# Kernel tuning notes

Hardware: AMD Instinct MI355X
Metric: run time of the kernel (lower is better)

The kernel has to match this reference:

```python
import jax, jax.numpy as jnp
from jax import lax
import numpy as np

B, T, F_IN, H = 64, 128, 12, 128  # batch, seq_len, input/output features, hidden


def _uinit(key, shape, fan):
    return jax.random.uniform(key, shape, jnp.float32, -1.0, 1.0) / np.float32(np.sqrt(fan))


def setup_inputs() -> dict:
    key = jax.random.key(0)
    ks = jax.random.split(key, 12)
    inp = {
        "x": jax.random.normal(ks[0], (B, T, F_IN), jnp.float32),
        # encoder LSTM (gate order i,f,g,o; b = b_ih + b_hh folded together)
        "enc_Wih": _uinit(ks[1], (4 * H, F_IN), H),
        "enc_Whh": _uinit(ks[2], (4 * H, H), H),
        "enc_b": _uinit(ks[3], (4 * H,), H),
        # decoder LSTM (input is the 12-dim teacher-forced x slice)
        "dec_Wih": _uinit(ks[4], (4 * H, F_IN), H),
        "dec_Whh": _uinit(ks[5], (4 * H, H), H),
        "dec_b": _uinit(ks[6], (4 * H,), H),
        # attention: Linear(2H -> H) with bias, then v: Linear(H -> 1, no bias)
        "attn_W": _uinit(ks[7], (H, 2 * H), 2 * H),
        "attn_b": _uinit(ks[8], (H,), 2 * H),
        "v_w": _uinit(ks[9], (H,), H),
        # output layer: Linear(2H -> F_IN)  (intended width; see notes)
        "out_W": _uinit(ks[10], (F_IN, 2 * H), 2 * H),
        "out_b": _uinit(ks[11], (F_IN,), 2 * H),
    }
    return inp


def _lstm_cell(xt, h, c, Wih, Whh, b):
    z = xt @ Wih.T + h @ Whh.T + b  # [B, 4H]
    i, f, g, o = jnp.split(z, 4, axis=-1)
    c = jax.nn.sigmoid(f) * c + jax.nn.sigmoid(i) * jnp.tanh(g)
    h = jax.nn.sigmoid(o) * jnp.tanh(c)
    return h, c


def reference(x, enc_Wih, enc_Whh, enc_b, dec_Wih, dec_Whh, dec_b,
              attn_W, attn_b, v_w, out_W, out_b):
    b_, t_, _ = x.shape
    hdim = enc_Whh.shape[1]
    xs = jnp.swapaxes(x, 0, 1)  # [T, B, F]
    h0 = jnp.zeros((b_, hdim), x.dtype)
    c0 = jnp.zeros((b_, hdim), x.dtype)

    def enc_step(carry, xt):
        h, c = carry
        h, c = _lstm_cell(xt, h, c, enc_Wih, enc_Whh, enc_b)
        return (h, c), h

    (hT, cT), enc_hs = lax.scan(enc_step, (h0, c0), xs)
    enc_out = jnp.swapaxes(enc_hs, 0, 1)  # [B, T, H]

    # split attn weight: cat(hidden, enc_out) @ W.T == hidden@W1.T + enc_out@W2.T
    W1, W2 = attn_W[:, :hdim], attn_W[:, hdim:]
    enc_proj = jnp.einsum("bth,gh->btg", enc_out, W2)  # precompute encoder side

    def dec_step(carry, xt):
        h, c = carry
        h, c = _lstm_cell(xt, h, c, dec_Wih, dec_Whh, dec_b)
        energy = jnp.tanh((h @ W1.T)[:, None, :] + enc_proj + attn_b)  # [B,T,H]
        score = jnp.einsum("bth,h->bt", energy, v_w)
        w = jax.nn.softmax(score, axis=1)  # attention over encoder time
        ctx = jnp.einsum("bt,bth->bh", w, enc_out)
        return (h, c), jnp.concatenate([h, ctx], axis=-1)  # [B, 2H]

    _, dec_ys = lax.scan(dec_step, (hT, cT), xs)
    dec_out = jnp.swapaxes(dec_ys, 0, 1)  # [B, T, 2H]
    return dec_out @ out_W.T + out_b  # [B, T, F]
```

## Files before the change

### kernel.cpp

```cpp
#include <hip/hip_runtime.h>
#include <hip/hip_bf16.h>

#define BB 64
#define TT 128
#define FIN 12
#define HH 128
#define GG 512

#define LOG2E 1.4426950408889634f
#define TWO_LOG2E 2.8853900817779268f

__device__ __forceinline__ float fexp2(float x) { return __builtin_amdgcn_exp2f(x); }
__device__ __forceinline__ float frcp(float x)  { return __builtin_amdgcn_rcpf(x); }

__device__ __forceinline__ float tanh_f(float x) {
  return 1.0f - 2.0f * frcp(1.0f + fexp2(TWO_LOG2E * x));
}
__device__ __forceinline__ float sigm_f(float x) {
  return frcp(1.0f + fexp2(-LOG2E * x));
}

template <int CTRL>
__device__ __forceinline__ float dpp_addstage(float v) {
  int s = __builtin_amdgcn_update_dpp(0, __float_as_int(v), CTRL, 0xF, 0xF, true);
  return v + __int_as_float(s);
}
__device__ __forceinline__ float red8(float v) {
  v = dpp_addstage<0xB1>(v);
  v = dpp_addstage<0x4E>(v);
  v = dpp_addstage<0x141>(v);
  return v;
}

#define FMA4S(acc, s, v) do { \
  acc.x = fmaf((s), (v).x, acc.x); \
  acc.y = fmaf((s), (v).y, acc.y); \
  acc.z = fmaf((s), (v).z, acc.z); \
  acc.w = fmaf((s), (v).w, acc.w); } while (0)

#define ACC4(hv, wv, a) do { \
  a = fmaf((hv).x, (wv).x, a); a = fmaf((hv).y, (wv).y, a); \
  a = fmaf((hv).z, (wv).z, a); a = fmaf((hv).w, (wv).w, a); } while (0)

__global__ __launch_bounds__(1024, 4) void lstm_kernel(
    const float* __restrict__ x,
    const float* __restrict__ eWih, const float* __restrict__ eWhh, const float* __restrict__ eb,
    const float* __restrict__ dWih, const float* __restrict__ dWhh, const float* __restrict__ db,
    float* __restrict__ encH, float* __restrict__ decH)
{
  const int b   = blockIdx.x;
  const int tid = threadIdx.x;
  const int q   = tid & 7;
  const int i   = tid >> 3;

  __shared__ __align__(16) float xs[TT * FIN];
  __shared__ __align__(16) float hbuf[2][160];
  __shared__ __align__(16) float hist[64 * HH];

  if (tid < (TT * FIN / 4))
    ((float4*)xs)[tid] = ((const float4*)(x + (size_t)b * TT * FIN))[tid];
  if (tid < 320) ((float*)hbuf)[tid] = 0.0f;
  float c = 0.0f;

  const int xo   = (q < 4) ? 3 * q : 0;
  const float xz = (q < 4) ? 1.0f : 0.0f;

  int ts = 0;
  #pragma unroll 1
  for (int phase = 0; phase < 2; ++phase) {
    const float* Wih  = phase ? dWih : eWih;
    const float* Whh  = phase ? dWhh : eWhh;
    const float* bias = phase ? db : eb;
    float* Hout       = phase ? decH : encH;

    float4 wg[4][4];
    #pragma unroll
    for (int g = 0; g < 4; ++g)
      #pragma unroll
      for (int j = 0; j < 4; ++j)
        wg[g][j] = *(const float4*)(Whh + ((g * HH + i) * HH) + 16 * q + 4 * j);

    float wx[4][3];
    #pragma unroll
    for (int g = 0; g < 4; ++g)
      #pragma unroll
      for (int j = 0; j < 3; ++j)
        wx[g][j] = Wih[(g * HH + i) * FIN + xo + j] * xz;

    const float bi = bias[i], bf = bias[HH + i], bg = bias[2 * HH + i], bo = bias[3 * HH + i];

    #pragma unroll 1
    for (int half = 0; half < 2; ++half) {
      #pragma unroll 1
      for (int tt = 0; tt < 64; ++tt, ++ts) {
        const int t = half * 64 + tt;
        __syncthreads();
        const float* hb = hbuf[ts & 1] + q * 20;
        float4 h0 = *(const float4*)(hb + 0);
        float4 h1 = *(const float4*)(hb + 4);
        float4 h2 = *(const float4*)(hb + 8);
        float4 h3 = *(const float4*)(hb + 12);

        const float* xt = xs + t * FIN + xo;
        float x0 = xt[0], x1 = xt[1], x2 = xt[2];
        float ai = wx[0][0] * x0 + wx[0][1] * x1 + wx[0][2] * x2;
        float af = wx[1][0] * x0 + wx[1][1] * x1 + wx[1][2] * x2;
        float ag = wx[2][0] * x0 + wx[2][1] * x1 + wx[2][2] * x2;
        float ao = wx[3][0] * x0 + wx[3][1] * x1 + wx[3][2] * x2;

        ACC4(h0, wg[0][0], ai); ACC4(h0, wg[1][0], af); ACC4(h0, wg[2][0], ag); ACC4(h0, wg[3][0], ao);
        ACC4(h1, wg[0][1], ai); ACC4(h1, wg[1][1], af); ACC4(h1, wg[2][1], ag); ACC4(h1, wg[3][1], ao);
        ACC4(h2, wg[0][2], ai); ACC4(h2, wg[1][2], af); ACC4(h2, wg[2][2], ag); ACC4(h2, wg[3][2], ao);
        ACC4(h3, wg[0][3], ai); ACC4(h3, wg[1][3], af); ACC4(h3, wg[2][3], ag); ACC4(h3, wg[3][3], ao);

        ai = red8(ai); af = red8(af); ag = red8(ag); ao = red8(ao);

        if (q == 0) {
          float zi = sigm_f(ai + bi);
          float zf = sigm_f(af + bf);
          float zg = tanh_f(ag + bg);
          float zo = sigm_f(ao + bo);
          c = fmaf(zf, c, zi * zg);
          float hn = zo * tanh_f(c);
          hbuf[(ts + 1) & 1][(i >> 4) * 20 + (i & 15)] = hn;
          hist[tt * HH + i] = hn;
        }
      }
      __syncthreads();
      {
        float4* dst = (float4*)(Hout + ((size_t)b * TT + half * 64) * HH);
        const float4* src = (const float4*)hist;
        dst[tid]        = src[tid];
        dst[tid + 1024] = src[tid + 1024];
      }
    }
  }
}

__global__ __launch_bounds__(256, 2) void proj_kernel(
    const float* __restrict__ encH, const float* __restrict__ decH,
    const float* __restrict__ attnW, const float* __restrict__ attnb,
    float* __restrict__ Abuf, float* __restrict__ Pbuf)
{
  const int m  = blockIdx.x & 1;
  const int b  = (blockIdx.x >> 1) & 63;
  const int r0 = (blockIdx.x >> 7) * 16;
  const int tid = threadIdx.x;

  __shared__ __align__(16) float WT[64 * 128];
  __shared__ __align__(16) float Xt[16 * 128];

  const float* X = (m ? encH : decH) + ((size_t)b * TT + r0) * HH;
  const float* W = attnW + (m ? HH : 0);

  ((float4*)Xt)[tid]       = ((const float4*)X)[tid];
  ((float4*)Xt)[256 + tid] = ((const float4*)X)[256 + tid];

  const int hq = tid & 31, rr = tid >> 5;
  const int h0 = 4 * hq;

  float4 acc0, acc1;
  if (m == 0) { acc0 = *(const float4*)(attnb + h0); acc1 = acc0; }
  else        { acc0 = make_float4(0.f, 0.f, 0.f, 0.f); acc1 = acc0; }

  for (int kb = 0; kb < 2; ++kb) {
    __syncthreads();
    {
      int h = tid >> 1, koff = (tid & 1) * 32;
      #pragma unroll
      for (int j = 0; j < 8; ++j) {
        float4 v = *(const float4*)(W + h * 256 + kb * 64 + koff + 4 * j);
        int kp = koff + 4 * j;
        WT[(kp + 0) * 128 + h] = v.x;
        WT[(kp + 1) * 128 + h] = v.y;
        WT[(kp + 2) * 128 + h] = v.z;
        WT[(kp + 3) * 128 + h] = v.w;
      }
    }
    __syncthreads();
    const float* xr0 = Xt + (2 * rr) * 128 + kb * 64;
    const float* xr1 = xr0 + 128;
    #pragma unroll
    for (int k4 = 0; k4 < 64; k4 += 4) {
      float4 xa = *(const float4*)(xr0 + k4);
      float4 xb = *(const float4*)(xr1 + k4);
      float4 w0 = *(const float4*)&WT[(k4 + 0) * 128 + h0];
      float4 w1 = *(const float4*)&WT[(k4 + 1) * 128 + h0];
      float4 w2 = *(const float4*)&WT[(k4 + 2) * 128 + h0];
      float4 w3 = *(const float4*)&WT[(k4 + 3) * 128 + h0];
      FMA4S(acc0, xa.x, w0); FMA4S(acc0, xa.y, w1);
      FMA4S(acc0, xa.z, w2); FMA4S(acc0, xa.w, w3);
      FMA4S(acc1, xb.x, w0); FMA4S(acc1, xb.y, w1);
      FMA4S(acc1, xb.z, w2); FMA4S(acc1, xb.w, w3);
    }
  }
  float* O = (m ? Pbuf : Abuf) + ((size_t)b * TT + r0) * HH;
  *(float4*)(O + (2 * rr) * 128 + h0)     = acc0;
  *(float4*)(O + (2 * rr + 1) * 128 + h0) = acc1;
}

__global__ __launch_bounds__(512, 2) void attn_kernel(
    const float* __restrict__ encH, const float* __restrict__ decH,
    const float* __restrict__ Abuf, const float* __restrict__ Pbuf,
    const float* __restrict__ vw, const float* __restrict__ outW,
    const float* __restrict__ outb, float* __restrict__ out)
{
  const int b  = blockIdx.x >> 3;
  const int s0 = (blockIdx.x & 7) * 16;
  const int tid = threadIdx.x;

  __shared__ __align__(16) float buf[64 * 128];
  __shared__ __align__(16) float a_lds[16 * 128];
  __shared__ __align__(16) float sc[16 * 128];
  __shared__ __align__(16) float dh[16 * 128];
  __shared__ __align__(16) float vl[HH];

  ((float4*)a_lds)[tid] = ((const float4*)(Abuf + ((size_t)b * TT + s0) * HH))[tid];
  ((float4*)dh)[tid]    = ((const float4*)(decH + ((size_t)b * TT + s0) * HH))[tid];
  if (tid < 32) ((float4*)vl)[tid] = ((const float4*)vw)[tid];

  const int u  = tid & 31;
  const int sl = tid >> 5;
  const int uq = u & 15;
  const int uh = u >> 4;

  for (int half = 0; half < 2; ++half) {
    const int tbase = half * 64;
    __syncthreads();
    #pragma unroll
    for (int i = 0; i < 4; ++i) {
      int flat = i * 2048 + tid * 4;
      int tp = flat >> 7;
      int h0 = flat & 127;
      float4 v = *(const float4*)(Pbuf + ((size_t)b * TT + tbase + tp) * HH + h0);
      int tq = tp >> 2, tr = tp & 3;
      buf[(h0 + 0) * 64 + 4 * ((tq ^ ((h0 + 0) >> 2)) & 15) + tr] = v.x;
      buf[(h0 + 1) * 64 + 4 * ((tq ^ ((h0 + 1) >> 2)) & 15) + tr] = v.y;
      buf[(h0 + 2) * 64 + 4 * ((tq ^ ((h0 + 2) >> 2)) & 15) + tr] = v.z;
      buf[(h0 + 3) * 64 + 4 * ((tq ^ ((h0 + 3) >> 2)) & 15) + tr] = v.w;
    }
    __syncthreads();
    float4 acc = make_float4(0.f, 0.f, 0.f, 0.f);
    const float* arow = a_lds + sl * 128;
    #pragma unroll 8
    for (int hh = 0; hh < 64; ++hh) {
      int h = uh * 64 + hh;
      float ah = arow[h];
      float vh = vl[h];
      float4 p4 = *(const float4*)&buf[h * 64 + 4 * ((uq ^ ((h >> 2) & 15)) & 15)];
      acc.x = fmaf(vh, tanh_f(ah + p4.x), acc.x);
      acc.y = fmaf(vh, tanh_f(ah + p4.y), acc.y);
      acc.z = fmaf(vh, tanh_f(ah + p4.z), acc.z);
      acc.w = fmaf(vh, tanh_f(ah + p4.w), acc.w);
    }
    acc.x += __shfl_xor(acc.x, 16, 64);
    acc.y += __shfl_xor(acc.y, 16, 64);
    acc.z += __shfl_xor(acc.z, 16, 64);
    acc.w += __shfl_xor(acc.w, 16, 64);
    if (uh == 0) *(float4*)&sc[sl * 128 + tbase + 4 * uq] = acc;
  }
  __syncthreads();

  {
    float4 sv = *(const float4*)&sc[sl * 128 + 4 * u];
    float mx = fmaxf(fmaxf(sv.x, sv.y), fmaxf(sv.z, sv.w));
    #pragma unroll
    for (int msk = 1; msk <= 16; msk <<= 1) mx = fmaxf(mx, __shfl_xor(mx, msk, 64));
    float4 e;
    e.x = fexp2(LOG2E * (sv.x - mx));
    e.y = fexp2(LOG2E * (sv.y - mx));
    e.z = fexp2(LOG2E * (sv.z - mx));
    e.w = fexp2(LOG2E * (sv.w - mx));
    float sm = (e.x + e.y) + (e.z + e.w);
    #pragma unroll
    for (int msk = 1; msk <= 16; msk <<= 1) sm += __shfl_xor(sm, msk, 64);
    float r = frcp(sm);
    e.x *= r; e.y *= r; e.z *= r; e.w *= r;
    *(float4*)&sc[sl * 128 + 4 * u] = e;
  }

  float4 ctx = make_float4(0.f, 0.f, 0.f, 0.f);
  const int h0c = 4 * u;
  for (int half = 0; half < 2; ++half) {
    const int tbase = half * 64;
    __syncthreads();
    #pragma unroll
    for (int i = 0; i < 4; ++i) {
      int flat = i * 2048 + tid * 4;
      int tp = flat >> 7;
      int hh0 = flat & 127;
      *(float4*)&buf[tp * 128 + hh0] =
          *(const float4*)(encH + ((size_t)b * TT + tbase + tp) * HH + hh0);
    }
    __syncthreads();
    const float* wrow = sc + sl * 128 + tbase;
    #pragma unroll 8
    for (int tp = 0; tp < 64; ++tp) {
      float wt = wrow[tp];
      float4 e4 = *(const float4*)&buf[tp * 128 + h0c];
      FMA4S(ctx, wt, e4);
    }
  }
  __syncthreads();
  *(float4*)&a_lds[sl * 128 + h0c] = ctx;
  __syncthreads();

  if (tid < 192) {
    int s = tid / 12, f = tid % 12;
    float acc = outb[f];
    const float4* w4 = (const float4*)(outW + f * 256);
    const float4* d4 = (const float4*)(dh + s * 128);
    const float4* c4 = (const float4*)(a_lds + s * 128);
    #pragma unroll
    for (int k = 0; k < 32; ++k) {
      float4 wv = w4[k], dv = d4[k];
      acc = fmaf(wv.x, dv.x, acc); acc = fmaf(wv.y, dv.y, acc);
      acc = fmaf(wv.z, dv.z, acc); acc = fmaf(wv.w, dv.w, acc);
    }
    #pragma unroll
    for (int k = 0; k < 32; ++k) {
      float4 wv = w4[32 + k], cv = c4[k];
      acc = fmaf(wv.x, cv.x, acc); acc = fmaf(wv.y, cv.y, acc);
      acc = fmaf(wv.z, cv.z, acc); acc = fmaf(wv.w, cv.w, acc);
    }
    out[((size_t)b * TT + s0 + s) * FIN + f] = acc;
  }
}

extern "C" void kernel_launch(void* const* d_in, const int* in_sizes, int n_in,
                              void* d_out, int out_size, void* d_ws, size_t ws_size,
                              hipStream_t stream)
{
  const float* x     = (const float*)d_in[0];
  const float* eWih  = (const float*)d_in[1];
  const float* eWhh  = (const float*)d_in[2];
  const float* eb    = (const float*)d_in[3];
  const float* dWih  = (const float*)d_in[4];
  const float* dWhh  = (const float*)d_in[5];
  const float* db    = (const float*)d_in[6];
  const float* attnW = (const float*)d_in[7];
  const float* attnb = (const float*)d_in[8];
  const float* vw    = (const float*)d_in[9];
  const float* outW  = (const float*)d_in[10];
  const float* outb  = (const float*)d_in[11];
  float* out = (float*)d_out;

  float* ws   = (float*)d_ws;
  const size_t SEG = (size_t)BB * TT * HH;
  float* encH = ws;
  float* decH = ws + SEG;
  float* Abuf = ws + 2 * SEG;
  float* Pbuf = ws + 3 * SEG;

  lstm_kernel<<<64, 1024, 0, stream>>>(x, eWih, eWhh, eb, dWih, dWhh, db, encH, decH);
  proj_kernel<<<1024, 256, 0, stream>>>(encH, decH, attnW, attnb, Abuf, Pbuf);
  attn_kernel<<<512, 512, 0, stream>>>(encH, decH, Abuf, Pbuf, vw, outW, outb, out);
}
```

Baseline: 338.8 us.

## Remap LSTM recurrence to one thread per gate row with quad broadcast

The recurrent LSTM kernel now assigns each of 512 threads a full gate row (128 weights held in registers) instead of splitting each hidden unit's four gates across 8 threads with DPP reductions. The cross-lane reduction is replaced by a single activation per thread, and the i/f/g/o values are then shared within each group of four lanes by DPP quad broadcasts. The intent is to shorten the serial per-timestep critical path (fewer reduction stages, parallel gate activations) and halve the block size. The cost is 128 weight registers per thread, which risks spills and lower occupancy, and every thread now reads the whole h vector from LDS (a broadcast read) each step.

```diff
diff --git a/kernel.cpp b/kernel.cpp
--- a/kernel.cpp
+++ b/kernel.cpp
@@ -21,15 +21,9 @@
 }
 
 template <int CTRL>
-__device__ __forceinline__ float dpp_addstage(float v) {
-  int s = __builtin_amdgcn_update_dpp(0, __float_as_int(v), CTRL, 0xF, 0xF, true);
-  return v + __int_as_float(s);
-}
-__device__ __forceinline__ float red8(float v) {
-  v = dpp_addstage<0xB1>(v);
-  v = dpp_addstage<0x4E>(v);
-  v = dpp_addstage<0x141>(v);
-  return v;
+__device__ __forceinline__ float quad_bcast(float v) {
+  return __int_as_float(
+      __builtin_amdgcn_update_dpp(0, __float_as_int(v), CTRL, 0xF, 0xF, true));
 }
 
 #define FMA4S(acc, s, v) do { \
@@ -42,7 +36,7 @@
   a = fmaf((hv).x, (wv).x, a); a = fmaf((hv).y, (wv).y, a); \
   a = fmaf((hv).z, (wv).z, a); a = fmaf((hv).w, (wv).w, a); } while (0)
 
-__global__ __launch_bounds__(1024, 4) void lstm_kernel(
+__global__ __launch_bounds__(512, 2) void lstm_kernel(
     const float* __restrict__ x,
     const float* __restrict__ eWih, const float* __restrict__ eWhh, const float* __restrict__ eb,
     const float* __restrict__ dWih, const float* __restrict__ dWhh, const float* __restrict__ db,
@@ -50,20 +44,20 @@
 {
   const int b   = blockIdx.x;
   const int tid = threadIdx.x;
-  const int q   = tid & 7;
-  const int i   = tid >> 3;
+  const int g   = tid & 3;
+  const int i   = tid >> 2;
 
   __shared__ __align__(16) float xs[TT * FIN];
-  __shared__ __align__(16) float hbuf[2][160];
+  __shared__ __align__(16) float hbuf[2][HH];
   __shared__ __align__(16) float hist[64 * HH];
 
   if (tid < (TT * FIN / 4))
     ((float4*)xs)[tid] = ((const float4*)(x + (size_t)b * TT * FIN))[tid];
-  if (tid < 320) ((float*)hbuf)[tid] = 0.0f;
+  if (tid < 256) ((float*)hbuf)[tid] = 0.0f;
   float c = 0.0f;
 
-  const int xo   = (q < 4) ? 3 * q : 0;
-  const float xz = (q < 4) ? 1.0f : 0.0f;
+  const bool isg = (g == 2);
+  const float mk = isg ? TWO_LOG2E : -LOG2E;
 
   int ts = 0;
   #pragma unroll 1
@@ -73,21 +67,16 @@
     const float* bias = phase ? db : eb;
     float* Hout       = phase ? decH : encH;
 
-    float4 wg[4][4];
-    #pragma unroll
-    for (int g = 0; g < 4; ++g)
-      #pragma unroll
-      for (int j = 0; j < 4; ++j)
-        wg[g][j] = *(const float4*)(Whh + ((g * HH + i) * HH) + 16 * q + 4 * j);
-
-    float wx[4][3];
-    #pragma unroll
-    for (int g = 0; g < 4; ++g)
-      #pragma unroll
-      for (int j = 0; j < 3; ++j)
-        wx[g][j] = Wih[(g * HH + i) * FIN + xo + j] * xz;
-
-    const float bi = bias[i], bf = bias[HH + i], bg = bias[2 * HH + i], bo = bias[3 * HH + i];
+    const int row = g * HH + i;
+    float4 wr[32];
+    #pragma unroll
+    for (int j = 0; j < 32; ++j)
+      wr[j] = *(const float4*)(Whh + (size_t)row * HH + 4 * j);
+
+    float4 wx0 = *(const float4*)(Wih + row * FIN + 0);
+    float4 wx1 = *(const float4*)(Wih + row * FIN + 4);
+    float4 wx2 = *(const float4*)(Wih + row * FIN + 8);
+    const float bb_ = bias[row];
 
     #pragma unroll 1
     for (int half = 0; half < 2; ++half) {
@@ -95,34 +84,42 @@
       for (int tt = 0; tt < 64; ++tt, ++ts) {
         const int t = half * 64 + tt;
         __syncthreads();
-        const float* hb = hbuf[ts & 1] + q * 20;
-        float4 h0 = *(const float4*)(hb + 0);
-        float4 h1 = *(const float4*)(hb + 4);
-        float4 h2 = *(const float4*)(hb + 8);
-        float4 h3 = *(const float4*)(hb + 12);
-
-        const float* xt = xs + t * FIN + xo;
-        float x0 = xt[0], x1 = xt[1], x2 = xt[2];
-        float ai = wx[0][0] * x0 + wx[0][1] * x1 + wx[0][2] * x2;
-        float af = wx[1][0] * x0 + wx[1][1] * x1 + wx[1][2] * x2;
-        float ag = wx[2][0] * x0 + wx[2][1] * x1 + wx[2][2] * x2;
-        float ao = wx[3][0] * x0 + wx[3][1] * x1 + wx[3][2] * x2;
-
-        ACC4(h0, wg[0][0], ai); ACC4(h0, wg[1][0], af); ACC4(h0, wg[2][0], ag); ACC4(h0, wg[3][0], ao);
-        ACC4(h1, wg[0][1], ai); ACC4(h1, wg[1][1], af); ACC4(h1, wg[2][1], ag); ACC4(h1, wg[3][1], ao);
-        ACC4(h2, wg[0][2], ai); ACC4(h2, wg[1][2], af); ACC4(h2, wg[2][2], ag); ACC4(h2, wg[3][2], ao);
-        ACC4(h3, wg[0][3], ai); ACC4(h3, wg[1][3], af); ACC4(h3, wg[2][3], ag); ACC4(h3, wg[3][3], ao);
-
-        ai = red8(ai); af = red8(af); ag = red8(ag); ao = red8(ao);
-
-        if (q == 0) {
-          float zi = sigm_f(ai + bi);
-          float zf = sigm_f(af + bf);
-          float zg = tanh_f(ag + bg);
-          float zo = sigm_f(ao + bo);
-          c = fmaf(zf, c, zi * zg);
-          float hn = zo * tanh_f(c);
-          hbuf[(ts + 1) & 1][(i >> 4) * 20 + (i & 15)] = hn;
+        const float* hb = hbuf[ts & 1];
+
+        float a0 = 0.f, a1 = 0.f, a2 = 0.f, a3 = 0.f;
+        #pragma unroll
+        for (int j = 0; j < 8; ++j) {
+          float4 h0 = *(const float4*)(hb + 16 * j + 0);
+          float4 h1 = *(const float4*)(hb + 16 * j + 4);
+          float4 h2 = *(const float4*)(hb + 16 * j + 8);
+          float4 h3 = *(const float4*)(hb + 16 * j + 12);
+          ACC4(h0, wr[4 * j + 0], a0);
+          ACC4(h1, wr[4 * j + 1], a1);
+          ACC4(h2, wr[4 * j + 2], a2);
+          ACC4(h3, wr[4 * j + 3], a3);
+        }
+        const float* xt = xs + t * FIN;
+        float4 xv0 = *(const float4*)(xt + 0);
+        float4 xv1 = *(const float4*)(xt + 4);
+        float4 xv2 = *(const float4*)(xt + 8);
+        ACC4(xv0, wx0, a0);
+        ACC4(xv1, wx1, a1);
+        ACC4(xv2, wx2, a2);
+
+        float a = ((a0 + a1) + (a2 + a3)) + bb_;
+
+        float r = frcp(1.0f + fexp2(mk * a));
+        float z = isg ? fmaf(-2.0f, r, 1.0f) : r;
+
+        float zi = quad_bcast<0x00>(z);
+        float zf = quad_bcast<0x55>(z);
+        float zg = quad_bcast<0xAA>(z);
+        float zo = quad_bcast<0xFF>(z);
+
+        c = fmaf(zf, c, zi * zg);
+        float hn = zo * tanh_f(c);
+        if (g == 0) {
+          hbuf[(ts + 1) & 1][i] = hn;
           hist[tt * HH + i] = hn;
         }
       }
@@ -131,7 +128,9 @@
         float4* dst = (float4*)(Hout + ((size_t)b * TT + half * 64) * HH);
         const float4* src = (const float4*)hist;
         dst[tid]        = src[tid];
+        dst[tid + 512]  = src[tid + 512];
         dst[tid + 1024] = src[tid + 1024];
+        dst[tid + 1536] = src[tid + 1536];
       }
     }
   }
@@ -352,7 +351,7 @@
   float* Abuf = ws + 2 * SEG;
   float* Pbuf = ws + 3 * SEG;
 
-  lstm_kernel<<<64, 1024, 0, stream>>>(x, eWih, eWhh, eb, dWih, dWhh, db, encH, decH);
+  lstm_kernel<<<64, 512, 0, stream>>>(x, eWih, eWhh, eb, dWih, dWhh, db, encH, decH);
   proj_kernel<<<1024, 256, 0, stream>>>(encH, decH, attnW, attnb, Abuf, Pbuf);
   attn_kernel<<<512, 512, 0, stream>>>(encH, decH, Abuf, Pbuf, vw, outW, outb, out);
 }
```

New measurement: 411.9 us. +21.6%, slower.

## Factor tanh exponentials into precomputed per-operand exp2 for attention energy

Applied to the files above, without the earlier changes.

Rewrites tanh(a+p) as 1 - 2/(1+e^{2a}·e^{2p}) and precomputes exp2 of both the decoder projection and the encoder projection once when they are loaded into LDS. The inner score loop then needs only one fma and one rcp per element instead of an exp2 per element. The constant term sum(v) is dropped because softmax is shift-invariant, and the score is scaled by -2. It also pads the a_lds/sc row stride to 132 and vectorizes the inner loop to read four h values per iteration. The cost is overflow risk when exp(2x) reaches inf for large projections, plus some accuracy loss.

```diff
diff --git a/kernel.cpp b/kernel.cpp
--- a/kernel.cpp
+++ b/kernel.cpp
@@ -199,6 +199,8 @@
   *(float4*)(O + (2 * rr + 1) * 128 + h0) = acc1;
 }
 
+#define AST 132
+
 __global__ __launch_bounds__(512, 2) void attn_kernel(
     const float* __restrict__ encH, const float* __restrict__ decH,
     const float* __restrict__ Abuf, const float* __restrict__ Pbuf,
@@ -210,13 +212,21 @@
   const int tid = threadIdx.x;
 
   __shared__ __align__(16) float buf[64 * 128];
-  __shared__ __align__(16) float a_lds[16 * 128];
-  __shared__ __align__(16) float sc[16 * 128];
+  __shared__ __align__(16) float a_lds[16 * AST];
+  __shared__ __align__(16) float sc[16 * AST];
   __shared__ __align__(16) float dh[16 * 128];
   __shared__ __align__(16) float vl[HH];
 
-  ((float4*)a_lds)[tid] = ((const float4*)(Abuf + ((size_t)b * TT + s0) * HH))[tid];
-  ((float4*)dh)[tid]    = ((const float4*)(decH + ((size_t)b * TT + s0) * HH))[tid];
+  {
+    int r = tid >> 5, c4 = (tid & 31) * 4;
+    float4 av = *(const float4*)(Abuf + ((size_t)b * TT + s0 + r) * HH + c4);
+    av.x = fexp2(TWO_LOG2E * av.x);
+    av.y = fexp2(TWO_LOG2E * av.y);
+    av.z = fexp2(TWO_LOG2E * av.z);
+    av.w = fexp2(TWO_LOG2E * av.w);
+    *(float4*)&a_lds[r * AST + c4] = av;
+  }
+  ((float4*)dh)[tid] = ((const float4*)(decH + ((size_t)b * TT + s0) * HH))[tid];
   if (tid < 32) ((float4*)vl)[tid] = ((const float4*)vw)[tid];
 
   const int u  = tid & 31;
@@ -233,6 +243,10 @@
       int tp = flat >> 7;
       int h0 = flat & 127;
       float4 v = *(const float4*)(Pbuf + ((size_t)b * TT + tbase + tp) * HH + h0);
+      v.x = fexp2(TWO_LOG2E * v.x);
+      v.y = fexp2(TWO_LOG2E * v.y);
+      v.z = fexp2(TWO_LOG2E * v.z);
+      v.w = fexp2(TWO_LOG2E * v.w);
       int tq = tp >> 2, tr = tp & 3;
       buf[(h0 + 0) * 64 + 4 * ((tq ^ ((h0 + 0) >> 2)) & 15) + tr] = v.x;
       buf[(h0 + 1) * 64 + 4 * ((tq ^ ((h0 + 1) >> 2)) & 15) + tr] = v.y;
@@ -241,28 +255,49 @@
     }
     __syncthreads();
     float4 acc = make_float4(0.f, 0.f, 0.f, 0.f);
-    const float* arow = a_lds + sl * 128;
-    #pragma unroll 8
-    for (int hh = 0; hh < 64; ++hh) {
-      int h = uh * 64 + hh;
-      float ah = arow[h];
-      float vh = vl[h];
-      float4 p4 = *(const float4*)&buf[h * 64 + 4 * ((uq ^ ((h >> 2) & 15)) & 15)];
-      acc.x = fmaf(vh, tanh_f(ah + p4.x), acc.x);
-      acc.y = fmaf(vh, tanh_f(ah + p4.y), acc.y);
-      acc.z = fmaf(vh, tanh_f(ah + p4.z), acc.z);
-      acc.w = fmaf(vh, tanh_f(ah + p4.w), acc.w);
+    const float* earow = a_lds + sl * AST;
+    #pragma unroll 4
+    for (int hh = 0; hh < 64; hh += 4) {
+      const int h = uh * 64 + hh;
+      float4 ea = *(const float4*)&earow[h];
+      float4 va = *(const float4*)&vl[h];
+      const int xoff = 4 * ((uq ^ ((h >> 2) & 15)) & 15);
+      float4 p0 = *(const float4*)&buf[(h + 0) * 64 + xoff];
+      float4 p1 = *(const float4*)&buf[(h + 1) * 64 + xoff];
+      float4 p2 = *(const float4*)&buf[(h + 2) * 64 + xoff];
+      float4 p3 = *(const float4*)&buf[(h + 3) * 64 + xoff];
+      acc.x = fmaf(va.x, frcp(fmaf(ea.x, p0.x, 1.f)), acc.x);
+      acc.y = fmaf(va.x, frcp(fmaf(ea.x, p0.y, 1.f)), acc.y);
+      acc.z = fmaf(va.x, frcp(fmaf(ea.x, p0.z, 1.f)), acc.z);
+      acc.w = fmaf(va.x, frcp(fmaf(ea.x, p0.w, 1.f)), acc.w);
+      acc.x = fmaf(va.y, frcp(fmaf(ea.y, p1.x, 1.f)), acc.x);
+      acc.y = fmaf(va.y, frcp(fmaf(ea.y, p1.y, 1.f)), acc.y);
+      acc.z = fmaf(va.y, frcp(fmaf(ea.y, p1.z, 1.f)), acc.z);
+      acc.w = fmaf(va.y, frcp(fmaf(ea.y, p1.w, 1.f)), acc.w);
+      acc.x = fmaf(va.z, frcp(fmaf(ea.z, p2.x, 1.f)), acc.x);
+      acc.y = fmaf(va.z, frcp(fmaf(ea.z, p2.y, 1.f)), acc.y);
+      acc.z = fmaf(va.z, frcp(fmaf(ea.z, p2.z, 1.f)), acc.z);
+      acc.w = fmaf(va.z, frcp(fmaf(ea.z, p2.w, 1.f)), acc.w);
+      acc.x = fmaf(va.w, frcp(fmaf(ea.w, p3.x, 1.f)), acc.x);
+      acc.y = fmaf(va.w, frcp(fmaf(ea.w, p3.y, 1.f)), acc.y);
+      acc.z = fmaf(va.w, frcp(fmaf(ea.w, p3.z, 1.f)), acc.z);
+      acc.w = fmaf(va.w, frcp(fmaf(ea.w, p3.w, 1.f)), acc.w);
     }
     acc.x += __shfl_xor(acc.x, 16, 64);
     acc.y += __shfl_xor(acc.y, 16, 64);
     acc.z += __shfl_xor(acc.z, 16, 64);
     acc.w += __shfl_xor(acc.w, 16, 64);
-    if (uh == 0) *(float4*)&sc[sl * 128 + tbase + 4 * uq] = acc;
+    if (uh == 0) {
+      float4 o;
+      o.x = -2.f * acc.x; o.y = -2.f * acc.y;
+      o.z = -2.f * acc.z; o.w = -2.f * acc.w;
+      *(float4*)&sc[sl * AST + tbase + 4 * uq] = o;
+    }
   }
   __syncthreads();
 
   {
-    float4 sv = *(const float4*)&sc[sl * 128 + 4 * u];
+    float4 sv = *(const float4*)&sc[sl * AST + 4 * u];
     float mx = fmaxf(fmaxf(sv.x, sv.y), fmaxf(sv.z, sv.w));
     #pragma unroll
     for (int msk = 1; msk <= 16; msk <<= 1) mx = fmaxf(mx, __shfl_xor(mx, msk, 64));
@@ -276,7 +311,7 @@
     for (int msk = 1; msk <= 16; msk <<= 1) sm += __shfl_xor(sm, msk, 64);
     float r = frcp(sm);
     e.x *= r; e.y *= r; e.z *= r; e.w *= r;
-    *(float4*)&sc[sl * 128 + 4 * u] = e;
+    *(float4*)&sc[sl * AST + 4 * u] = e;
   }
 
   float4 ctx = make_float4(0.f, 0.f, 0.f, 0.f);
@@ -293,7 +328,7 @@
           *(const float4*)(encH + ((size_t)b * TT + tbase + tp) * HH + hh0);
     }
     __syncthreads();
-    const float* wrow = sc + sl * 128 + tbase;
+    const float* wrow = sc + sl * AST + tbase;
     #pragma unroll 8
     for (int tp = 0; tp < 64; ++tp) {
       float wt = wrow[tp];
@@ -302,7 +337,7 @@
     }
   }
   __syncthreads();
-  *(float4*)&a_lds[sl * 128 + h0c] = ctx;
+  *(float4*)&a_lds[sl * AST + h0c] = ctx;
   __syncthreads();
 
   if (tid < 192) {
@@ -310,7 +345,7 @@
     float acc = outb[f];
     const float4* w4 = (const float4*)(outW + f * 256);
     const float4* d4 = (const float4*)(dh + s * 128);
-    const float4* c4 = (const float4*)(a_lds + s * 128);
+    const float4* c4 = (const float4*)(a_lds + s * AST);
     #pragma unroll
     for (int k = 0; k < 32; ++k) {
       float4 wv = w4[k], dv = d4[k];
```

New measurement: 322.3 us. 4.9% less time.
